# Kernel optimization log

Hardware: AMD Instinct MI355X
Metric: run time of the kernel (lower is better)

Reference implementation:

```python
import jax, jax.numpy as jnp
import numpy as np

D_IN = 1280
D = 256
NPF = (D // 3 // 2) * 2  # 84 sine features per coordinate
PAD = D - NPF * 3        # 4
_EPS = 1e-6


def pos_embed_sine(xyz):
    # PositionEmbeddingCoordsSine(n_dim=3, d_model=256, scale=1.0)
    dim_t = jnp.arange(NPF, dtype=jnp.float32)
    dim_t = 10000.0 ** (2.0 * jnp.floor(dim_t / 2.0) / NPF)
    x = xyz * (2.0 * np.pi)                       # scale * 2*pi
    pd = x[..., None] / dim_t                     # (..., 3, 84)
    emb = jnp.stack([jnp.sin(pd[..., 0::2]), jnp.cos(pd[..., 1::2])], axis=-1)
    emb = emb.reshape(*xyz.shape[:-1], -1)        # (..., 252)
    pad_cfg = [(0, 0)] * (xyz.ndim - 1) + [(0, PAD)]
    return jnp.pad(emb, pad_cfg)                  # (..., 256)


def compute_rigid_transform(a, b, w):
    # weighted Kabsch / Procrustes, batched 3x3 SVD (faithful to torch source)
    wn = w[..., None] / jnp.maximum(jnp.sum(w, axis=-1, keepdims=True)[..., None], _EPS)
    ca = jnp.sum(a * wn, axis=-2)                 # (B, 3)
    cb = jnp.sum(b * wn, axis=-2)
    ac = a - ca[..., None, :]
    bc = b - cb[..., None, :]
    cov = jnp.swapaxes(ac, -2, -1) @ (bc * wn)    # (B, 3, 3)
    u, s, vh = jnp.linalg.svd(cov)
    v = jnp.swapaxes(vh, -2, -1)
    ut = jnp.swapaxes(u, -2, -1)
    rot_pos = v @ ut
    v_neg = v.at[..., 2].multiply(-1.0)           # negate 3rd column of V
    rot_neg = v_neg @ ut
    rot = jnp.where(jnp.linalg.det(rot_pos)[..., None, None] > 0, rot_pos, rot_neg)
    t = -rot @ ca[..., :, None] + cb[..., :, None]
    return jnp.concatenate([rot, t], axis=-1)     # (B, 3, 4)


def setup_inputs() -> dict:
    key = jax.random.key(0)
    ks = jax.random.split(key, 12)
    B, N = 16, 2048
    feat1 = jax.random.normal(ks[0], (B, N, D_IN), dtype=jnp.float32)
    xyz1 = jax.random.normal(ks[1], (B, N, 3), dtype=jnp.float32)
    feat2 = jax.random.normal(ks[2], (B, N, D_IN), dtype=jnp.float32)
    xyz2 = jax.random.normal(ks[3], (B, N, 3), dtype=jnp.float32)
    s_in = 1.0 / np.sqrt(D_IN)
    s_d = 1.0 / np.sqrt(D)
    Wf = jax.random.normal(ks[4], (D_IN, D), dtype=jnp.float32) * s_in
    bf = jnp.zeros((D,), dtype=jnp.float32)
    Wq = jax.random.normal(ks[5], (D, D), dtype=jnp.float32) * s_d
    bq = jnp.zeros((D,), dtype=jnp.float32)
    Wk = jax.random.normal(ks[6], (D, D), dtype=jnp.float32) * s_d
    bk = jnp.zeros((D,), dtype=jnp.float32)
    Wc = jax.random.normal(ks[7], (D, 1), dtype=jnp.float32) * s_d
    bc = jnp.zeros((1,), dtype=jnp.float32)
    return {"feat1": feat1, "xyz1": xyz1, "feat2": feat2, "xyz2": xyz2,
            "Wf": Wf, "bf": bf, "Wq": Wq, "bq": bq, "Wk": Wk, "bk": bk,
            "Wc": Wc, "bc": bc}


def reference(feat1, xyz1, feat2, xyz2, Wf, bf, Wq, bq, Wk, bk, Wc, bc):
    # project features to embed dim (feat_proj)
    srcf = feat1 @ Wf + bf                        # (B, Ns, 256)
    tgtf = feat2 @ Wf + bf                        # (B, Nt, 256)
    # add sinusoidal positional embeddings (use_pos_emb=True)
    src2 = srcf + pos_embed_sine(xyz1)
    tgt2 = tgtf + pos_embed_sine(xyz2)
    # simple_attention: project q, k only; value is raw xyz
    scale = 1.0 / np.sqrt(D)
    qs = (src2 @ Wq + bq) * scale
    kt = tgt2 @ Wk + bk
    attn_st = jax.nn.softmax(jnp.einsum('bqd,bsd->bqs', qs, kt), axis=-1)
    src_corr = jnp.einsum('bqs,bsc->bqc', attn_st, xyz2)   # (B, Ns, 3)
    qt = (tgt2 @ Wq + bq) * scale
    ks_ = src2 @ Wk + bk
    attn_ts = jax.nn.softmax(jnp.einsum('bqd,bsd->bqs', qt, ks_), axis=-1)
    tgt_corr = jnp.einsum('bqs,bsc->bqc', attn_ts, xyz1)   # (B, Nt, 3)
    # overlap confidence logits -> sigmoid weights in [0, 1]
    src_w = jax.nn.sigmoid((srcf @ Wc + bc)[..., 0])       # (B, Ns)
    tgt_w = jax.nn.sigmoid((tgtf @ Wc + bc)[..., 0])       # (B, Nt)
    # weighted rigid transform from pooled correspondences
    a = jnp.concatenate([xyz1, tgt_corr], axis=1)
    b = jnp.concatenate([src_corr, xyz2], axis=1)
    w = jnp.concatenate([src_w, tgt_w], axis=1)
    return compute_rigid_transform(a, b, w)                # (B, 3, 4)
```

## Files before the change

kernel.cpp:

```cpp
#include <hip/hip_runtime.h>
#include <math.h>

#define NB 16
#define NPTS 2048
#define DIN 1280
#define DM 256
#define BNROWS (NB * NPTS)

typedef __attribute__((ext_vector_type(8))) short bf16x8;
typedef __attribute__((ext_vector_type(4))) float f32x4;

static __device__ __forceinline__ ushort f2bf(float f) {
    uint x = __float_as_uint(f);
    return (ushort)((x + 0x7FFF + ((x >> 16) & 1)) >> 16);
}

static __device__ __forceinline__ uint cvtpk(float lo, float hi) {
    uint r;
    asm("v_cvt_pk_bf16_f32 %0, %1, %2" : "=v"(r) : "v"(lo), "v"(hi));
    return r;
}

__global__ __launch_bounds__(256)
void convert_wt(const float* __restrict__ W, ushort* __restrict__ Wt,
                const int K, const int N)
{
    const int idx = blockIdx.x * 256 + threadIdx.x;
    if (idx >= K * N) return;
    const int n = idx / K, k = idx - n * K;
    Wt[idx] = f2bf(W[(size_t)k * N + n]);
}

__global__ __launch_bounds__(256)
void proj_mfma(const float* __restrict__ A, const ushort* __restrict__ Wt,
               const float* __restrict__ bias, const float* __restrict__ Wc,
               const float* __restrict__ xyz, ushort* __restrict__ out,
               float* __restrict__ logits)
{
    __shared__ ushort Al[64 * 32];
    __shared__ float invfreq[42];
    const int t = threadIdx.x;
    const int lane = t & 63, w = t >> 6;
    const int col15 = lane & 15, sub = lane >> 4;
    const int m0 = blockIdx.x * 64;

    if (t < 42) invfreq[t] = __expf((float)(2 * t) * (-9.210340371976184f / 84.0f));

    f32x4 acc[4][4];
    #pragma unroll
    for (int s = 0; s < 4; ++s)
        #pragma unroll
        for (int u = 0; u < 4; ++u) acc[s][u] = (f32x4){0.f, 0.f, 0.f, 0.f};

    const float* Ag = A + (size_t)(m0 + (t >> 2)) * DIN + (t & 3) * 8;
    const ushort* Wg[4];
    #pragma unroll
    for (int u = 0; u < 4; ++u)
        Wg[u] = Wt + (size_t)(w * 64 + u * 16 + col15) * DIN + sub * 8;

    for (int k0 = 0; k0 < DIN; k0 += 32) {
        const float4 a0 = *(const float4*)(Ag + k0);
        const float4 a1 = *(const float4*)(Ag + k0 + 4);
        uint p[4];
        p[0] = cvtpk(a0.x, a0.y); p[1] = cvtpk(a0.z, a0.w);
        p[2] = cvtpk(a1.x, a1.y); p[3] = cvtpk(a1.z, a1.w);
        __syncthreads();
        *(uint4*)(Al + t * 8) = *(uint4*)p;
        __syncthreads();
        bf16x8 bfr[4];
        #pragma unroll
        for (int u = 0; u < 4; ++u) bfr[u] = *(const bf16x8*)(Wg[u] + k0);
        #pragma unroll
        for (int s = 0; s < 4; ++s) {
            const bf16x8 af = *(const bf16x8*)(Al + (s * 16 + col15) * 32 + sub * 8);
            #pragma unroll
            for (int u = 0; u < 4; ++u)
                acc[s][u] = __builtin_amdgcn_mfma_f32_16x16x32_bf16(af, bfr[u], acc[s][u], 0, 0, 0);
        }
    }

    float bias_u[4], wc_u[4];
    int   cidx[4];
    #pragma unroll
    for (int u = 0; u < 4; ++u) {
        cidx[u]  = w * 64 + u * 16 + col15;
        bias_u[u] = bias[cidx[u]];
        wc_u[u]   = Wc[cidx[u]];
    }
    #pragma unroll
    for (int s = 0; s < 4; ++s) {
        #pragma unroll
        for (int r = 0; r < 4; ++r) {
            const int row = m0 + s * 16 + sub * 4 + r;
            const float px = xyz[(size_t)row * 3 + 0];
            const float py = xyz[(size_t)row * 3 + 1];
            const float pz = xyz[(size_t)row * 3 + 2];
            float wp = 0.f;
            #pragma unroll
            for (int u = 0; u < 4; ++u) {
                const int c = cidx[u];
                const float val = acc[s][u][r] + bias_u[u];
                wp = fmaf(val, wc_u[u], wp);
                float pv = 0.f;
                if (c < 252) {
                    const int coord = c / 84;
                    const int f = c - coord * 84;
                    const float xc = (coord == 0) ? px : ((coord == 1) ? py : pz);
                    const float vv = xc * 6.283185307179586f * invfreq[f >> 1];
                    pv = (f & 1) ? __cosf(vv) : __sinf(vv);
                }
                out[(size_t)row * DM + c] = f2bf(val + pv);
            }
            wp += __shfl_xor(wp, 1); wp += __shfl_xor(wp, 2);
            wp += __shfl_xor(wp, 4); wp += __shfl_xor(wp, 8);
            if (col15 == 0) atomicAdd(&logits[row], wp);
        }
    }
}

__global__ __launch_bounds__(256)
void qk_mfma(const ushort* __restrict__ A, const ushort* __restrict__ Wt,
             const float* __restrict__ bias, const float alpha,
             ushort* __restrict__ out)
{
    __shared__ ushort Al[64 * 32];
    const int t = threadIdx.x;
    const int lane = t & 63, w = t >> 6;
    const int col15 = lane & 15, sub = lane >> 4;
    const int m0 = blockIdx.x * 64;

    f32x4 acc[4][4];
    #pragma unroll
    for (int s = 0; s < 4; ++s)
        #pragma unroll
        for (int u = 0; u < 4; ++u) acc[s][u] = (f32x4){0.f, 0.f, 0.f, 0.f};

    const ushort* Ag = A + (size_t)(m0 + (t >> 2)) * DM + (t & 3) * 8;
    const ushort* Wg[4];
    #pragma unroll
    for (int u = 0; u < 4; ++u)
        Wg[u] = Wt + (size_t)(w * 64 + u * 16 + col15) * DM + sub * 8;

    for (int k0 = 0; k0 < DM; k0 += 32) {
        const uint4 av = *(const uint4*)(Ag + k0);
        __syncthreads();
        *(uint4*)(Al + t * 8) = av;
        __syncthreads();
        bf16x8 bfr[4];
        #pragma unroll
        for (int u = 0; u < 4; ++u) bfr[u] = *(const bf16x8*)(Wg[u] + k0);
        #pragma unroll
        for (int s = 0; s < 4; ++s) {
            const bf16x8 af = *(const bf16x8*)(Al + (s * 16 + col15) * 32 + sub * 8);
            #pragma unroll
            for (int u = 0; u < 4; ++u)
                acc[s][u] = __builtin_amdgcn_mfma_f32_16x16x32_bf16(af, bfr[u], acc[s][u], 0, 0, 0);
        }
    }

    float bias_u[4];
    int cidx[4];
    #pragma unroll
    for (int u = 0; u < 4; ++u) {
        cidx[u] = w * 64 + u * 16 + col15;
        bias_u[u] = bias[cidx[u]];
    }
    #pragma unroll
    for (int s = 0; s < 4; ++s)
        #pragma unroll
        for (int r = 0; r < 4; ++r) {
            const int row = m0 + s * 16 + sub * 4 + r;
            #pragma unroll
            for (int u = 0; u < 4; ++u)
                out[(size_t)row * DM + cidx[u]] = f2bf((acc[s][u][r] + bias_u[u]) * alpha);
        }
}

__global__ __launch_bounds__(256)
void sigmoid_kernel(float* __restrict__ w, const float* __restrict__ bc, int n)
{
    const int i = blockIdx.x * 256 + threadIdx.x;
    if (i < n) {
        const float z = w[i] + bc[0];
        w[i] = 1.0f / (1.0f + expf(-z));
    }
}

__global__ __launch_bounds__(256, 2)
void attn_mfma(const ushort* __restrict__ Q, const ushort* __restrict__ K,
               const float* __restrict__ V, float* __restrict__ acc4)
{
    const int b    = blockIdx.y;
    const int lane = threadIdx.x & 63;
    const int wv   = threadIdx.x >> 6;
    const int col  = lane & 15;
    const int sub  = lane >> 4;
    const int qbase = blockIdx.x * 256 + wv * 64;
    const int k0    = blockIdx.z * 512;

    const ushort* Qb = Q + (size_t)b * NPTS * DM;
    const ushort* Kb = K + (size_t)b * NPTS * DM;
    const float*  Vb = V + (size_t)b * NPTS * 3;

    bf16x8 aq[4][8];
    #pragma unroll
    for (int s = 0; s < 4; ++s) {
        const ushort* qrow = Qb + (size_t)(qbase + s * 16 + col) * DM + sub * 8;
        #pragma unroll
        for (int c = 0; c < 8; ++c)
            aq[s][c] = *(const bf16x8*)(qrow + c * 32);
    }

    float lsum[4][4], ax[4][4], ay[4][4], az[4][4];
    #pragma unroll
    for (int s = 0; s < 4; ++s)
        #pragma unroll
        for (int r = 0; r < 4; ++r) {
            lsum[s][r] = 0.f; ax[s][r] = 0.f; ay[s][r] = 0.f; az[s][r] = 0.f;
        }

    for (int kt = k0; kt < k0 + 512; kt += 16) {
        const ushort* krow = Kb + (size_t)(kt + col) * DM + sub * 8;
        f32x4 sv0 = {0.f, 0.f, 0.f, 0.f};
        f32x4 sv1 = {0.f, 0.f, 0.f, 0.f};
        f32x4 sv2 = {0.f, 0.f, 0.f, 0.f};
        f32x4 sv3 = {0.f, 0.f, 0.f, 0.f};
        #pragma unroll
        for (int c = 0; c < 8; ++c) {
            const bf16x8 bk = *(const bf16x8*)(krow + c * 32);
            sv0 = __builtin_amdgcn_mfma_f32_16x16x32_bf16(aq[0][c], bk, sv0, 0, 0, 0);
            sv1 = __builtin_amdgcn_mfma_f32_16x16x32_bf16(aq[1][c], bk, sv1, 0, 0, 0);
            sv2 = __builtin_amdgcn_mfma_f32_16x16x32_bf16(aq[2][c], bk, sv2, 0, 0, 0);
            sv3 = __builtin_amdgcn_mfma_f32_16x16x32_bf16(aq[3][c], bk, sv3, 0, 0, 0);
        }
        const float vx = Vb[(size_t)(kt + col) * 3 + 0];
        const float vy = Vb[(size_t)(kt + col) * 3 + 1];
        const float vz = Vb[(size_t)(kt + col) * 3 + 2];
        #pragma unroll
        for (int r = 0; r < 4; ++r) {
            const float p0 = __expf(sv0[r] - 16.0f);
            const float p1 = __expf(sv1[r] - 16.0f);
            const float p2 = __expf(sv2[r] - 16.0f);
            const float p3 = __expf(sv3[r] - 16.0f);
            lsum[0][r] += p0; ax[0][r] = fmaf(p0, vx, ax[0][r]);
            ay[0][r] = fmaf(p0, vy, ay[0][r]); az[0][r] = fmaf(p0, vz, az[0][r]);
            lsum[1][r] += p1; ax[1][r] = fmaf(p1, vx, ax[1][r]);
            ay[1][r] = fmaf(p1, vy, ay[1][r]); az[1][r] = fmaf(p1, vz, az[1][r]);
            lsum[2][r] += p2; ax[2][r] = fmaf(p2, vx, ax[2][r]);
            ay[2][r] = fmaf(p2, vy, ay[2][r]); az[2][r] = fmaf(p2, vz, az[2][r]);
            lsum[3][r] += p3; ax[3][r] = fmaf(p3, vx, ax[3][r]);
            ay[3][r] = fmaf(p3, vy, ay[3][r]); az[3][r] = fmaf(p3, vz, az[3][r]);
        }
    }

    #pragma unroll
    for (int off = 1; off < 16; off <<= 1) {
        #pragma unroll
        for (int s = 0; s < 4; ++s)
            #pragma unroll
            for (int r = 0; r < 4; ++r) {
                lsum[s][r] += __shfl_xor(lsum[s][r], off);
                ax[s][r]   += __shfl_xor(ax[s][r], off);
                ay[s][r]   += __shfl_xor(ay[s][r], off);
                az[s][r]   += __shfl_xor(az[s][r], off);
            }
    }
    if (col == 0) {
        #pragma unroll
        for (int s = 0; s < 4; ++s)
            #pragma unroll
            for (int r = 0; r < 4; ++r) {
                const int row = qbase + s * 16 + sub * 4 + r;
                float* dst = acc4 + ((size_t)b * NPTS + row) * 4;
                atomicAdd(dst + 0, lsum[s][r]);
                atomicAdd(dst + 1, ax[s][r]);
                atomicAdd(dst + 2, ay[s][r]);
                atomicAdd(dst + 3, az[s][r]);
            }
    }
}

__global__ __launch_bounds__(256)
void reduce_kernel(const float* __restrict__ xyz1, const float* __restrict__ xyz2,
                   const float* __restrict__ sacc, const float* __restrict__ tacc,
                   const float* __restrict__ srcw, const float* __restrict__ tgtw,
                   double* __restrict__ bsums)
{
    const int b = blockIdx.x;
    const int t = threadIdx.x;
    double s[16];
    #pragma unroll
    for (int k = 0; k < 16; ++k) s[k] = 0.0;

    for (int i = t; i < 2 * NPTS; i += 256) {
        float ax_, ay_, az_, bx_, by_, bz_, w;
        if (i < NPTS) {
            const size_t row = (size_t)b * NPTS + i;
            ax_ = xyz1[row * 3]; ay_ = xyz1[row * 3 + 1]; az_ = xyz1[row * 3 + 2];
            const float4 s4 = *(const float4*)(sacc + row * 4);
            const float inv = 1.0f / s4.x;
            bx_ = s4.y * inv; by_ = s4.z * inv; bz_ = s4.w * inv;
            w = srcw[row];
        } else {
            const size_t row = (size_t)b * NPTS + (i - NPTS);
            const float4 t4 = *(const float4*)(tacc + row * 4);
            const float inv = 1.0f / t4.x;
            ax_ = t4.y * inv; ay_ = t4.z * inv; az_ = t4.w * inv;
            bx_ = xyz2[row * 3]; by_ = xyz2[row * 3 + 1]; bz_ = xyz2[row * 3 + 2];
            w = tgtw[row];
        }
        const double dw = (double)w;
        const double dax = ax_, day = ay_, daz = az_;
        const double dbx = bx_, dby = by_, dbz = bz_;
        s[0] += dw;
        s[1] += dw * dax; s[2] += dw * day; s[3] += dw * daz;
        s[4] += dw * dbx; s[5] += dw * dby; s[6] += dw * dbz;
        s[7]  += dw * dax * dbx; s[8]  += dw * dax * dby; s[9]  += dw * dax * dbz;
        s[10] += dw * day * dbx; s[11] += dw * day * dby; s[12] += dw * day * dbz;
        s[13] += dw * daz * dbx; s[14] += dw * daz * dby; s[15] += dw * daz * dbz;
    }

    __shared__ double red[256][16];
    #pragma unroll
    for (int k = 0; k < 16; ++k) red[t][k] = s[k];
    __syncthreads();
    for (int step = 128; step >= 1; step >>= 1) {
        if (t < step) {
            #pragma unroll
            for (int k = 0; k < 16; ++k) red[t][k] += red[t + step][k];
        }
        __syncthreads();
    }
    if (t == 0) {
        #pragma unroll
        for (int k = 0; k < 16; ++k) bsums[b * 16 + k] = red[0][k];
    }
}

__global__ void svd_kernel(const double* __restrict__ bsums, float* __restrict__ out)
{
    const int b = threadIdx.x;
    if (b >= NB) return;
    const double* s = bsums + b * 16;
    double Wd = s[0];
    if (Wd < 1e-6) Wd = 1e-6;
    const double inv = 1.0 / Wd;

    double ca[3], cb[3];
    for (int r = 0; r < 3; ++r) { ca[r] = s[1 + r] * inv; cb[r] = s[4 + r] * inv; }
    double cov[3][3];
    for (int r = 0; r < 3; ++r)
        for (int c = 0; c < 3; ++c)
            cov[r][c] = s[7 + r * 3 + c] * inv - ca[r] * cb[c];

    double Mm[3][3];
    for (int i = 0; i < 3; ++i)
        for (int j = 0; j < 3; ++j)
            Mm[i][j] = cov[0][i] * cov[0][j] + cov[1][i] * cov[1][j] + cov[2][i] * cov[2][j];

    double Vm[3][3] = {{1, 0, 0}, {0, 1, 0}, {0, 0, 1}};
    const int PP[3] = {0, 0, 1}, QQ[3] = {1, 2, 2};
    for (int sweep = 0; sweep < 20; ++sweep) {
        for (int pi = 0; pi < 3; ++pi) {
            const int p = PP[pi], q = QQ[pi];
            const double apq = Mm[p][q];
            if (fabs(apq) < 1e-300) continue;
            const double tau = (Mm[q][q] - Mm[p][p]) / (2.0 * apq);
            const double tt = ((tau >= 0.0) ? 1.0 : -1.0) / (fabs(tau) + sqrt(1.0 + tau * tau));
            const double c = 1.0 / sqrt(1.0 + tt * tt);
            const double sn = tt * c;
            for (int k = 0; k < 3; ++k) {
                const double mkp = Mm[k][p], mkq = Mm[k][q];
                Mm[k][p] = c * mkp - sn * mkq;
                Mm[k][q] = sn * mkp + c * mkq;
            }
            for (int k = 0; k < 3; ++k) {
                const double mpk = Mm[p][k], mqk = Mm[q][k];
                Mm[p][k] = c * mpk - sn * mqk;
                Mm[q][k] = sn * mpk + c * mqk;
            }
            for (int k = 0; k < 3; ++k) {
                const double vkp = Vm[k][p], vkq = Vm[k][q];
                Vm[k][p] = c * vkp - sn * vkq;
                Vm[k][q] = sn * vkp + c * vkq;
            }
        }
    }

    double l0 = Mm[0][0], l1 = Mm[1][1], l2 = Mm[2][2];
    double v0[3], v1[3], v2[3];
    for (int k = 0; k < 3; ++k) { v0[k] = Vm[k][0]; v1[k] = Vm[k][1]; v2[k] = Vm[k][2]; }
    if (l0 < l1) { double tmp = l0; l0 = l1; l1 = tmp;
        for (int k = 0; k < 3; ++k) { double tv = v0[k]; v0[k] = v1[k]; v1[k] = tv; } }
    if (l0 < l2) { double tmp = l0; l0 = l2; l2 = tmp;
        for (int k = 0; k < 3; ++k) { double tv = v0[k]; v0[k] = v2[k]; v2[k] = tv; } }
    if (l1 < l2) { double tmp = l1; l1 = l2; l2 = tmp;
        for (int k = 0; k < 3; ++k) { double tv = v1[k]; v1[k] = v2[k]; v2[k] = tv; } }

    double u0[3], u1[3], u2[3];
    for (int r = 0; r < 3; ++r) u0[r] = cov[r][0] * v0[0] + cov[r][1] * v0[1] + cov[r][2] * v0[2];
    for (int r = 0; r < 3; ++r) u1[r] = cov[r][0] * v1[0] + cov[r][1] * v1[1] + cov[r][2] * v1[2];
    double n0 = sqrt(u0[0] * u0[0] + u0[1] * u0[1] + u0[2] * u0[2]);
    if (n0 > 1e-30) { for (int k = 0; k < 3; ++k) u0[k] /= n0; }
    else { u0[0] = 1; u0[1] = 0; u0[2] = 0; }
    const double d01 = u0[0] * u1[0] + u0[1] * u1[1] + u0[2] * u1[2];
    for (int k = 0; k < 3; ++k) u1[k] -= d01 * u0[k];
    double n1 = sqrt(u1[0] * u1[0] + u1[1] * u1[1] + u1[2] * u1[2]);
    if (n1 > 1e-30) { for (int k = 0; k < 3; ++k) u1[k] /= n1; }
    else {
        const double aa0 = fabs(u0[0]), aa1 = fabs(u0[1]), aa2 = fabs(u0[2]);
        const int ax = (aa0 <= aa1 && aa0 <= aa2) ? 0 : ((aa1 <= aa2) ? 1 : 2);
        double e[3] = {0, 0, 0}; e[ax] = 1.0;
        const double d = u0[ax];
        for (int k = 0; k < 3; ++k) u1[k] = e[k] - d * u0[k];
        const double nn = sqrt(u1[0] * u1[0] + u1[1] * u1[1] + u1[2] * u1[2]);
        for (int k = 0; k < 3; ++k) u1[k] /= nn;
    }
    u2[0] = u0[1] * u1[2] - u0[2] * u1[1];
    u2[1] = u0[2] * u1[0] - u0[0] * u1[2];
    u2[2] = u0[0] * u1[1] - u0[1] * u1[0];

    double R[3][3];
    for (int r = 0; r < 3; ++r)
        for (int c = 0; c < 3; ++c)
            R[r][c] = v0[r] * u0[c] + v1[r] * u1[c] + v2[r] * u2[c];
    const double det = R[0][0] * (R[1][1] * R[2][2] - R[1][2] * R[2][1])
                     - R[0][1] * (R[1][0] * R[2][2] - R[1][2] * R[2][0])
                     + R[0][2] * (R[1][0] * R[2][1] - R[1][1] * R[2][0]);
    if (det <= 0.0) {
        for (int r = 0; r < 3; ++r)
            for (int c = 0; c < 3; ++c)
                R[r][c] -= 2.0 * v2[r] * u2[c];
    }
    double tv[3];
    for (int r = 0; r < 3; ++r)
        tv[r] = cb[r] - (R[r][0] * ca[0] + R[r][1] * ca[1] + R[r][2] * ca[2]);

    for (int r = 0; r < 3; ++r) {
        out[b * 12 + r * 4 + 0] = (float)R[r][0];
        out[b * 12 + r * 4 + 1] = (float)R[r][1];
        out[b * 12 + r * 4 + 2] = (float)R[r][2];
        out[b * 12 + r * 4 + 3] = (float)tv[r];
    }
}

extern "C" void kernel_launch(void* const* d_in, const int* in_sizes, int n_in,
                              void* d_out, int out_size, void* d_ws, size_t ws_size,
                              hipStream_t stream)
{
    const float* feat1 = (const float*)d_in[0];
    const float* xyz1  = (const float*)d_in[1];
    const float* feat2 = (const float*)d_in[2];
    const float* xyz2  = (const float*)d_in[3];
    const float* Wf = (const float*)d_in[4];
    const float* bf = (const float*)d_in[5];
    const float* Wq = (const float*)d_in[6];
    const float* bq = (const float*)d_in[7];
    const float* Wk = (const float*)d_in[8];
    const float* bk = (const float*)d_in[9];
    const float* Wc = (const float*)d_in[10];
    const float* bc = (const float*)d_in[11];
    float* out = (float*)d_out;

    float*  srcw = (float*)d_ws;
    float*  tgtw = srcw + BNROWS;
    float*  sacc = tgtw + BNROWS;
    float*  tacc = sacc + (size_t)BNROWS * 4;
    double* bsums = (double*)(tacc + (size_t)BNROWS * 4);
    ushort* src2 = (ushort*)(bsums + NB * 16);
    ushort* tgt2 = src2 + (size_t)BNROWS * DM;
    ushort* qbuf = tgt2 + (size_t)BNROWS * DM;
    ushort* kbuf = qbuf + (size_t)BNROWS * DM;
    ushort* wft  = kbuf + (size_t)BNROWS * DM;
    ushort* wqt  = wft + 256 * 1280;
    ushort* wkt  = wqt + 256 * 256;

    hipMemsetAsync(d_ws, 0, (size_t)10 * BNROWS * sizeof(float), stream);

    convert_wt<<<(DIN * DM) / 256, 256, 0, stream>>>(Wf, wft, DIN, DM);
    convert_wt<<<(DM * DM) / 256, 256, 0, stream>>>(Wq, wqt, DM, DM);
    convert_wt<<<(DM * DM) / 256, 256, 0, stream>>>(Wk, wkt, DM, DM);

    const dim3 gm(BNROWS / 64);
    proj_mfma<<<gm, 256, 0, stream>>>(feat1, wft, bf, Wc, xyz1, src2, srcw);
    proj_mfma<<<gm, 256, 0, stream>>>(feat2, wft, bf, Wc, xyz2, tgt2, tgtw);
    sigmoid_kernel<<<(2 * BNROWS) / 256, 256, 0, stream>>>(srcw, bc, 2 * BNROWS);

    const float scale = 1.0f / 16.0f;
    const dim3 gattn(NPTS / 256, NB, 4);

    qk_mfma<<<gm, 256, 0, stream>>>(src2, wqt, bq, scale, qbuf);
    qk_mfma<<<gm, 256, 0, stream>>>(tgt2, wkt, bk, 1.0f, kbuf);
    attn_mfma<<<gattn, 256, 0, stream>>>(qbuf, kbuf, xyz2, sacc);

    qk_mfma<<<gm, 256, 0, stream>>>(tgt2, wqt, bq, scale, qbuf);
    qk_mfma<<<gm, 256, 0, stream>>>(src2, wkt, bk, 1.0f, kbuf);
    attn_mfma<<<gattn, 256, 0, stream>>>(qbuf, kbuf, xyz1, tacc);

    reduce_kernel<<<NB, 256, 0, stream>>>(xyz1, xyz2, sacc, tacc, srcw, tgtw, bsums);
    svd_kernel<<<1, 64, 0, stream>>>(bsums, out);
}
```

Baseline: 759.5 us.

## Prefetch operands, swizzle LDS, retile attention, parallelize reduction and fold log2e into Q

The projection GEMMs now double-buffer their next A and W fragments in registers and XOR-swizzle the LDS tile to avoid bank conflicts. The attention kernel halves the query rows per wave, doubles the key splits, and ping-pongs K fragments so the next tile loads while MFMAs run. It also uses exp2 with log2e folded into the Q scale. The reduction runs across 16 blocks per batch with double atomics, the weight transpose writes coalesced reads, and Jacobi sweeps drop from 20 to 8. Risks include atomic ordering nondeterminism and fewer SVD sweeps possibly reducing accuracy.

Result: slower. 899.8 us (+18.5%).

```diff
diff --git a/kernel.cpp b/kernel.cpp
--- a/kernel.cpp
+++ b/kernel.cpp
@@ -10,6 +10,8 @@
 typedef __attribute__((ext_vector_type(8))) short bf16x8;
 typedef __attribute__((ext_vector_type(4))) float f32x4;
 
+#define SHIFT2 23.083120654223414f
+
 static __device__ __forceinline__ ushort f2bf(float f) {
     uint x = __float_as_uint(f);
     return (ushort)((x + 0x7FFF + ((x >> 16) & 1)) >> 16);
@@ -27,8 +29,8 @@
 {
     const int idx = blockIdx.x * 256 + threadIdx.x;
     if (idx >= K * N) return;
-    const int n = idx / K, k = idx - n * K;
-    Wt[idx] = f2bf(W[(size_t)k * N + n]);
+    const int k = idx / N, n = idx - k * N;
+    Wt[(size_t)n * K + k] = f2bf(W[idx]);
 }
 
 __global__ __launch_bounds__(256)
@@ -58,25 +60,39 @@
     for (int u = 0; u < 4; ++u)
         Wg[u] = Wt + (size_t)(w * 64 + u * 16 + col15) * DIN + sub * 8;
 
+    char* const lds_w = (char*)Al + ((t * 16) ^ ((((t >> 2) >> 1) & 3) << 4));
+    const int rd_sw = (((col15 >> 1) & 3) << 4);
+
+    float4 a0 = *(const float4*)(Ag);
+    float4 a1 = *(const float4*)(Ag + 4);
+    bf16x8 bcur[4];
+    #pragma unroll
+    for (int u = 0; u < 4; ++u) bcur[u] = *(const bf16x8*)(Wg[u]);
+
+    #pragma unroll 2
     for (int k0 = 0; k0 < DIN; k0 += 32) {
-        const float4 a0 = *(const float4*)(Ag + k0);
-        const float4 a1 = *(const float4*)(Ag + k0 + 4);
         uint p[4];
         p[0] = cvtpk(a0.x, a0.y); p[1] = cvtpk(a0.z, a0.w);
         p[2] = cvtpk(a1.x, a1.y); p[3] = cvtpk(a1.z, a1.w);
         __syncthreads();
-        *(uint4*)(Al + t * 8) = *(uint4*)p;
+        *(uint4*)lds_w = *(uint4*)p;
         __syncthreads();
-        bf16x8 bfr[4];
-        #pragma unroll
-        for (int u = 0; u < 4; ++u) bfr[u] = *(const bf16x8*)(Wg[u] + k0);
+        const int kn = (k0 + 32 < DIN) ? (k0 + 32) : 0;
+        a0 = *(const float4*)(Ag + kn);
+        a1 = *(const float4*)(Ag + kn + 4);
+        bf16x8 bnext[4];
+        #pragma unroll
+        for (int u = 0; u < 4; ++u) bnext[u] = *(const bf16x8*)(Wg[u] + kn);
         #pragma unroll
         for (int s = 0; s < 4; ++s) {
-            const bf16x8 af = *(const bf16x8*)(Al + (s * 16 + col15) * 32 + sub * 8);
+            const bf16x8 af = *(const bf16x8*)((const char*)Al +
+                (((s * 16 + col15) * 64 + sub * 16) ^ rd_sw));
             #pragma unroll
             for (int u = 0; u < 4; ++u)
-                acc[s][u] = __builtin_amdgcn_mfma_f32_16x16x32_bf16(af, bfr[u], acc[s][u], 0, 0, 0);
-        }
+                acc[s][u] = __builtin_amdgcn_mfma_f32_16x16x32_bf16(af, bcur[u], acc[s][u], 0, 0, 0);
+        }
+        #pragma unroll
+        for (int u = 0; u < 4; ++u) bcur[u] = bnext[u];
     }
 
     float bias_u[4], wc_u[4];
@@ -141,21 +157,34 @@
     for (int u = 0; u < 4; ++u)
         Wg[u] = Wt + (size_t)(w * 64 + u * 16 + col15) * DM + sub * 8;
 
+    char* const lds_w = (char*)Al + ((t * 16) ^ ((((t >> 2) >> 1) & 3) << 4));
+    const int rd_sw = (((col15 >> 1) & 3) << 4);
+
+    uint4 av = *(const uint4*)(Ag);
+    bf16x8 bcur[4];
+    #pragma unroll
+    for (int u = 0; u < 4; ++u) bcur[u] = *(const bf16x8*)(Wg[u]);
+
+    #pragma unroll 2
     for (int k0 = 0; k0 < DM; k0 += 32) {
-        const uint4 av = *(const uint4*)(Ag + k0);
         __syncthreads();
-        *(uint4*)(Al + t * 8) = av;
+        *(uint4*)lds_w = av;
         __syncthreads();
-        bf16x8 bfr[4];
-        #pragma unroll
-        for (int u = 0; u < 4; ++u) bfr[u] = *(const bf16x8*)(Wg[u] + k0);
+        const int kn = (k0 + 32 < DM) ? (k0 + 32) : 0;
+        av = *(const uint4*)(Ag + kn);
+        bf16x8 bnext[4];
+        #pragma unroll
+        for (int u = 0; u < 4; ++u) bnext[u] = *(const bf16x8*)(Wg[u] + kn);
         #pragma unroll
         for (int s = 0; s < 4; ++s) {
-            const bf16x8 af = *(const bf16x8*)(Al + (s * 16 + col15) * 32 + sub * 8);
+            const bf16x8 af = *(const bf16x8*)((const char*)Al +
+                (((s * 16 + col15) * 64 + sub * 16) ^ rd_sw));
             #pragma unroll
             for (int u = 0; u < 4; ++u)
-                acc[s][u] = __builtin_amdgcn_mfma_f32_16x16x32_bf16(af, bfr[u], acc[s][u], 0, 0, 0);
-        }
+                acc[s][u] = __builtin_amdgcn_mfma_f32_16x16x32_bf16(af, bcur[u], acc[s][u], 0, 0, 0);
+        }
+        #pragma unroll
+        for (int u = 0; u < 4; ++u) bcur[u] = bnext[u];
     }
 
     float bias_u[4];
@@ -183,6 +212,39 @@
     if (i < n) {
         const float z = w[i] + bc[0];
         w[i] = 1.0f / (1.0f + expf(-z));
+    }
+}
+
+static __device__ __forceinline__ void attn_body(
+    const bf16x8 aq0[8], const bf16x8 aq1[8],
+    const bf16x8 kcur[8], const float vx, const float vy, const float vz,
+    bf16x8 knext[8], float& nvx, float& nvy, float& nvz,
+    const ushort* __restrict__ Kb, const float* __restrict__ Vb,
+    const int ktn, const int col, const int sub,
+    float lsum[2][4], float ax[2][4], float ay[2][4], float az[2][4])
+{
+    const ushort* kr = Kb + (size_t)(ktn + col) * DM + sub * 8;
+    #pragma unroll
+    for (int c = 0; c < 8; ++c) knext[c] = *(const bf16x8*)(kr + c * 32);
+    nvx = Vb[(size_t)(ktn + col) * 3 + 0];
+    nvy = Vb[(size_t)(ktn + col) * 3 + 1];
+    nvz = Vb[(size_t)(ktn + col) * 3 + 2];
+
+    f32x4 sv0 = {0.f, 0.f, 0.f, 0.f};
+    f32x4 sv1 = {0.f, 0.f, 0.f, 0.f};
+    #pragma unroll
+    for (int c = 0; c < 8; ++c) {
+        sv0 = __builtin_amdgcn_mfma_f32_16x16x32_bf16(aq0[c], kcur[c], sv0, 0, 0, 0);
+        sv1 = __builtin_amdgcn_mfma_f32_16x16x32_bf16(aq1[c], kcur[c], sv1, 0, 0, 0);
+    }
+    #pragma unroll
+    for (int r = 0; r < 4; ++r) {
+        const float p0 = exp2f(sv0[r] - SHIFT2);
+        const float p1 = exp2f(sv1[r] - SHIFT2);
+        lsum[0][r] += p0; ax[0][r] = fmaf(p0, vx, ax[0][r]);
+        ay[0][r] = fmaf(p0, vy, ay[0][r]); az[0][r] = fmaf(p0, vz, az[0][r]);
+        lsum[1][r] += p1; ax[1][r] = fmaf(p1, vx, ax[1][r]);
+        ay[1][r] = fmaf(p1, vy, ay[1][r]); az[1][r] = fmaf(p1, vz, az[1][r]);
     }
 }
 
@@ -195,68 +257,56 @@
     const int wv   = threadIdx.x >> 6;
     const int col  = lane & 15;
     const int sub  = lane >> 4;
-    const int qbase = blockIdx.x * 256 + wv * 64;
-    const int k0    = blockIdx.z * 512;
+    const int qbase = blockIdx.x * 128 + wv * 32;
+    const int k0    = blockIdx.z * 256;
 
     const ushort* Qb = Q + (size_t)b * NPTS * DM;
     const ushort* Kb = K + (size_t)b * NPTS * DM;
     const float*  Vb = V + (size_t)b * NPTS * 3;
 
-    bf16x8 aq[4][8];
-    #pragma unroll
-    for (int s = 0; s < 4; ++s) {
-        const ushort* qrow = Qb + (size_t)(qbase + s * 16 + col) * DM + sub * 8;
-        #pragma unroll
-        for (int c = 0; c < 8; ++c)
-            aq[s][c] = *(const bf16x8*)(qrow + c * 32);
-    }
-
-    float lsum[4][4], ax[4][4], ay[4][4], az[4][4];
-    #pragma unroll
-    for (int s = 0; s < 4; ++s)
+    bf16x8 aq0[8], aq1[8];
+    {
+        const ushort* q0 = Qb + (size_t)(qbase + col) * DM + sub * 8;
+        const ushort* q1 = Qb + (size_t)(qbase + 16 + col) * DM + sub * 8;
+        #pragma unroll
+        for (int c = 0; c < 8; ++c) {
+            aq0[c] = *(const bf16x8*)(q0 + c * 32);
+            aq1[c] = *(const bf16x8*)(q1 + c * 32);
+        }
+    }
+
+    float lsum[2][4], ax[2][4], ay[2][4], az[2][4];
+    #pragma unroll
+    for (int s = 0; s < 2; ++s)
         #pragma unroll
         for (int r = 0; r < 4; ++r) {
             lsum[s][r] = 0.f; ax[s][r] = 0.f; ay[s][r] = 0.f; az[s][r] = 0.f;
         }
 
-    for (int kt = k0; kt < k0 + 512; kt += 16) {
-        const ushort* krow = Kb + (size_t)(kt + col) * DM + sub * 8;
-        f32x4 sv0 = {0.f, 0.f, 0.f, 0.f};
-        f32x4 sv1 = {0.f, 0.f, 0.f, 0.f};
-        f32x4 sv2 = {0.f, 0.f, 0.f, 0.f};
-        f32x4 sv3 = {0.f, 0.f, 0.f, 0.f};
-        #pragma unroll
-        for (int c = 0; c < 8; ++c) {
-            const bf16x8 bk = *(const bf16x8*)(krow + c * 32);
-            sv0 = __builtin_amdgcn_mfma_f32_16x16x32_bf16(aq[0][c], bk, sv0, 0, 0, 0);
-            sv1 = __builtin_amdgcn_mfma_f32_16x16x32_bf16(aq[1][c], bk, sv1, 0, 0, 0);
-            sv2 = __builtin_amdgcn_mfma_f32_16x16x32_bf16(aq[2][c], bk, sv2, 0, 0, 0);
-            sv3 = __builtin_amdgcn_mfma_f32_16x16x32_bf16(aq[3][c], bk, sv3, 0, 0, 0);
-        }
-        const float vx = Vb[(size_t)(kt + col) * 3 + 0];
-        const float vy = Vb[(size_t)(kt + col) * 3 + 1];
-        const float vz = Vb[(size_t)(kt + col) * 3 + 2];
-        #pragma unroll
-        for (int r = 0; r < 4; ++r) {
-            const float p0 = __expf(sv0[r] - 16.0f);
-            const float p1 = __expf(sv1[r] - 16.0f);
-            const float p2 = __expf(sv2[r] - 16.0f);
-            const float p3 = __expf(sv3[r] - 16.0f);
-            lsum[0][r] += p0; ax[0][r] = fmaf(p0, vx, ax[0][r]);
-            ay[0][r] = fmaf(p0, vy, ay[0][r]); az[0][r] = fmaf(p0, vz, az[0][r]);
-            lsum[1][r] += p1; ax[1][r] = fmaf(p1, vx, ax[1][r]);
-            ay[1][r] = fmaf(p1, vy, ay[1][r]); az[1][r] = fmaf(p1, vz, az[1][r]);
-            lsum[2][r] += p2; ax[2][r] = fmaf(p2, vx, ax[2][r]);
-            ay[2][r] = fmaf(p2, vy, ay[2][r]); az[2][r] = fmaf(p2, vz, az[2][r]);
-            lsum[3][r] += p3; ax[3][r] = fmaf(p3, vx, ax[3][r]);
-            ay[3][r] = fmaf(p3, vy, ay[3][r]); az[3][r] = fmaf(p3, vz, az[3][r]);
-        }
+    bf16x8 kbA[8], kbB[8];
+    float vxA, vyA, vzA, vxB, vyB, vzB;
+    {
+        const ushort* kr = Kb + (size_t)(k0 + col) * DM + sub * 8;
+        #pragma unroll
+        for (int c = 0; c < 8; ++c) kbA[c] = *(const bf16x8*)(kr + c * 32);
+        vxA = Vb[(size_t)(k0 + col) * 3 + 0];
+        vyA = Vb[(size_t)(k0 + col) * 3 + 1];
+        vzA = Vb[(size_t)(k0 + col) * 3 + 2];
+    }
+
+    for (int kt = k0; kt < k0 + 256; kt += 32) {
+        attn_body(aq0, aq1, kbA, vxA, vyA, vzA, kbB, vxB, vyB, vzB,
+                  Kb, Vb, kt + 16, col, sub, lsum, ax, ay, az);
+        int kt2 = kt + 32;
+        if (kt2 >= k0 + 256) kt2 = k0;
+        attn_body(aq0, aq1, kbB, vxB, vyB, vzB, kbA, vxA, vyA, vzA,
+                  Kb, Vb, kt2, col, sub, lsum, ax, ay, az);
     }
 
     #pragma unroll
     for (int off = 1; off < 16; off <<= 1) {
         #pragma unroll
-        for (int s = 0; s < 4; ++s)
+        for (int s = 0; s < 2; ++s)
             #pragma unroll
             for (int r = 0; r < 4; ++r) {
                 lsum[s][r] += __shfl_xor(lsum[s][r], off);
@@ -267,7 +317,7 @@
     }
     if (col == 0) {
         #pragma unroll
-        for (int s = 0; s < 4; ++s)
+        for (int s = 0; s < 2; ++s)
             #pragma unroll
             for (int r = 0; r < 4; ++r) {
                 const int row = qbase + s * 16 + sub * 4 + r;
@@ -288,11 +338,12 @@
 {
     const int b = blockIdx.x;
     const int t = threadIdx.x;
+    const int i = blockIdx.y * 256 + t;
     double s[16];
     #pragma unroll
     for (int k = 0; k < 16; ++k) s[k] = 0.0;
 
-    for (int i = t; i < 2 * NPTS; i += 256) {
+    {
         float ax_, ay_, az_, bx_, by_, bz_, w;
         if (i < NPTS) {
             const size_t row = (size_t)b * NPTS + i;
@@ -312,12 +363,12 @@
         const double dw = (double)w;
         const double dax = ax_, day = ay_, daz = az_;
         const double dbx = bx_, dby = by_, dbz = bz_;
-        s[0] += dw;
-        s[1] += dw * dax; s[2] += dw * day; s[3] += dw * daz;
-        s[4] += dw * dbx; s[5] += dw * dby; s[6] += dw * dbz;
-        s[7]  += dw * dax * dbx; s[8]  += dw * dax * dby; s[9]  += dw * dax * dbz;
-        s[10] += dw * day * dbx; s[11] += dw * day * dby; s[12] += dw * day * dbz;
-        s[13] += dw * daz * dbx; s[14] += dw * daz * dby; s[15] += dw * daz * dbz;
+        s[0] = dw;
+        s[1] = dw * dax; s[2] = dw * day; s[3] = dw * daz;
+        s[4] = dw * dbx; s[5] = dw * dby; s[6] = dw * dbz;
+        s[7]  = dw * dax * dbx; s[8]  = dw * dax * dby; s[9]  = dw * dax * dbz;
+        s[10] = dw * day * dbx; s[11] = dw * day * dby; s[12] = dw * day * dbz;
+        s[13] = dw * daz * dbx; s[14] = dw * daz * dby; s[15] = dw * daz * dbz;
     }
 
     __shared__ double red[256][16];
@@ -333,7 +384,7 @@
     }
     if (t == 0) {
         #pragma unroll
-        for (int k = 0; k < 16; ++k) bsums[b * 16 + k] = red[0][k];
+        for (int k = 0; k < 16; ++k) atomicAdd(&bsums[b * 16 + k], red[0][k]);
     }
 }
 
@@ -360,7 +411,7 @@
 
     double Vm[3][3] = {{1, 0, 0}, {0, 1, 0}, {0, 0, 1}};
     const int PP[3] = {0, 0, 1}, QQ[3] = {1, 2, 2};
-    for (int sweep = 0; sweep < 20; ++sweep) {
+    for (int sweep = 0; sweep < 8; ++sweep) {
         for (int pi = 0; pi < 3; ++pi) {
             const int p = PP[pi], q = QQ[pi];
             const double apq = Mm[p][q];
@@ -475,7 +526,7 @@
     ushort* wqt  = wft + 256 * 1280;
     ushort* wkt  = wqt + 256 * 256;
 
-    hipMemsetAsync(d_ws, 0, (size_t)10 * BNROWS * sizeof(float), stream);
+    hipMemsetAsync(d_ws, 0, (size_t)10 * BNROWS * sizeof(float) + NB * 16 * sizeof(double), stream);
 
     convert_wt<<<(DIN * DM) / 256, 256, 0, stream>>>(Wf, wft, DIN, DM);
     convert_wt<<<(DM * DM) / 256, 256, 0, stream>>>(Wq, wqt, DM, DM);
@@ -486,17 +537,17 @@
     proj_mfma<<<gm, 256, 0, stream>>>(feat2, wft, bf, Wc, xyz2, tgt2, tgtw);
     sigmoid_kernel<<<(2 * BNROWS) / 256, 256, 0, stream>>>(srcw, bc, 2 * BNROWS);
 
-    const float scale = 1.0f / 16.0f;
-    const dim3 gattn(NPTS / 256, NB, 4);
-
-    qk_mfma<<<gm, 256, 0, stream>>>(src2, wqt, bq, scale, qbuf);
+    const float alphaQ = 1.4426950408889634f / 16.0f;
+    const dim3 gattn(NPTS / 128, NB, 8);
+
+    qk_mfma<<<gm, 256, 0, stream>>>(src2, wqt, bq, alphaQ, qbuf);
     qk_mfma<<<gm, 256, 0, stream>>>(tgt2, wkt, bk, 1.0f, kbuf);
     attn_mfma<<<gattn, 256, 0, stream>>>(qbuf, kbuf, xyz2, sacc);
 
-    qk_mfma<<<gm, 256, 0, stream>>>(tgt2, wqt, bq, scale, qbuf);
+    qk_mfma<<<gm, 256, 0, stream>>>(tgt2, wqt, bq, alphaQ, qbuf);
     qk_mfma<<<gm, 256, 0, stream>>>(src2, wkt, bk, 1.0f, kbuf);
     attn_mfma<<<gattn, 256, 0, stream>>>(qbuf, kbuf, xyz1, tacc);
 
-    reduce_kernel<<<NB, 256, 0, stream>>>(xyz1, xyz2, sacc, tacc, srcw, tgtw, bsums);
+    reduce_kernel<<<dim3(NB, 16), 256, 0, stream>>>(xyz1, xyz2, sacc, tacc, srcw, tgtw, bsums);
     svd_kernel<<<1, 64, 0, stream>>>(bsums, out);
 }
```
